# Kernel optimization log

Measured on AMD Instinct MI355X. Metric: run time of the kernel, lower is better.

Reference implementation:

```python
import jax, jax.numpy as jnp
import numpy as np

ALPHA = 1.0  # DPMConfig.alpha
N, D, K = 4096, 256, 64


def setup_inputs() -> dict:
    key = jax.random.key(0)
    k1, k2, k3, k4 = jax.random.split(key, 4)
    x = jax.random.normal(k1, (N, D), dtype=jnp.float32)
    means = jax.random.normal(k2, (K, D), dtype=jnp.float32)
    # SPD covariances: A A^T / D + 0.5 I
    A = jax.random.normal(k3, (K, D, D), dtype=jnp.float32)
    covs = jnp.einsum('kde,kfe->kdf', A, A) / D + 0.5 * jnp.eye(D, dtype=jnp.float32)
    counts = jax.random.uniform(k4, (K,), dtype=jnp.float32, minval=1.0, maxval=200.0)
    n_points = 100000
    return {"x": x, "means": means, "covs": covs, "counts": counts, "n_points": n_points}


def reference(x, means, covs, counts, n_points):
    n, d = x.shape
    k = means.shape[0]
    # deviations from every cluster mean: [N, K, D]
    dev = x[:, None, :] - means[None, :, :]
    # batched Mahalanobis solve: covs broadcast over points
    solved = jnp.linalg.solve(covs[None], dev[..., None])[..., 0]  # [N, K, D]
    quad = jnp.sum(dev * solved, axis=-1)  # [N, K]
    # logdet with the same jitter as the original
    _, log_dets = jnp.linalg.slogdet(covs + 1e-10 * jnp.eye(d, dtype=covs.dtype))  # [K]
    log_lik = -0.5 * (d * jnp.log(2.0 * jnp.pi) + log_dets[None, :] + quad)  # [N, K]
    denom = jnp.asarray(n_points, jnp.float32) + ALPHA
    log_prior = jnp.log(counts / denom)  # [K]
    log_new = jnp.log(ALPHA / denom)
    log_probs = jnp.concatenate(
        [log_lik + log_prior[None, :], jnp.full((n, 1), log_new, dtype=x.dtype)], axis=1
    )  # [N, K+1]
    # stable normalize (max-subtract + exp + sum == softmax)
    probs = jax.nn.softmax(log_probs, axis=1)
    return probs
```

## Files before the change

### kernel.cpp

```cpp
#include <hip/hip_runtime.h>
#include <math.h>


#define DD 256
#define KC 64
#define NPTS 4096
#define NT 64
#define BB 64
#define KG 4

__global__ __launch_bounds__(512) void pivot_kernel(
    const float* __restrict__ covs, float* __restrict__ S,
    float* __restrict__ Plbuf, float* __restrict__ ldp, int bs)
{
  const int k = blockIdx.x;
  const int by = blockIdx.y;
  const int tid = threadIdx.x;
  float* Pb = Plbuf + (size_t)k * BB * BB;

  __shared__ __align__(16) float Tl[BB][BB + 4];
  __shared__ __align__(16) float pivc[2][BB];
  __shared__ __align__(16) float pivr[2][BB];

  if (by < 4) {
    if (bs == 0) return;
    const int j0p = (bs - 1) * BB;
    const int r0 = by * BB;
    const float* src = ((bs == 1) ? covs : (const float*)S) + (size_t)k * DD * DD;
    float* dst = S + (size_t)k * DD * DD;

    const int rr = tid >> 3;
    const int cc = (tid & 7) * 8;
    *reinterpret_cast<float4*>(&Tl[rr][cc]) =
        *reinterpret_cast<const float4*>(&Pb[rr * BB + cc]);
    *reinterpret_cast<float4*>(&Tl[rr][cc + 4]) =
        *reinterpret_cast<const float4*>(&Pb[rr * BB + cc + 4]);
    __syncthreads();

    const int r = r0 + rr;
    if (r0 == j0p) {
      *reinterpret_cast<float4*>(&dst[(size_t)r * DD + j0p + cc]) =
          *reinterpret_cast<const float4*>(&Tl[rr][cc]);
      *reinterpret_cast<float4*>(&dst[(size_t)r * DD + j0p + cc + 4]) =
          *reinterpret_cast<const float4*>(&Tl[rr][cc + 4]);
    } else {
      float Crow[BB];
      #pragma unroll
      for (int p = 0; p < BB; p += 4) {
        float4 cv = *reinterpret_cast<const float4*>(&src[(size_t)r * DD + j0p + p]);
        Crow[p] = cv.x; Crow[p + 1] = cv.y; Crow[p + 2] = cv.z; Crow[p + 3] = cv.w;
      }
      float acc[8] = {0.f, 0.f, 0.f, 0.f, 0.f, 0.f, 0.f, 0.f};
      #pragma unroll
      for (int p = 0; p < BB; ++p) {
        float4 t0 = *reinterpret_cast<const float4*>(&Tl[p][cc]);
        float4 t1 = *reinterpret_cast<const float4*>(&Tl[p][cc + 4]);
        acc[0] = fmaf(Crow[p], t0.x, acc[0]);
        acc[1] = fmaf(Crow[p], t0.y, acc[1]);
        acc[2] = fmaf(Crow[p], t0.z, acc[2]);
        acc[3] = fmaf(Crow[p], t0.w, acc[3]);
        acc[4] = fmaf(Crow[p], t1.x, acc[4]);
        acc[5] = fmaf(Crow[p], t1.y, acc[5]);
        acc[6] = fmaf(Crow[p], t1.z, acc[6]);
        acc[7] = fmaf(Crow[p], t1.w, acc[7]);
      }
      float4 o0 = {-acc[0], -acc[1], -acc[2], -acc[3]};
      float4 o1 = {-acc[4], -acc[5], -acc[6], -acc[7]};
      *reinterpret_cast<float4*>(&dst[(size_t)r * DD + j0p + cc]) = o0;
      *reinterpret_cast<float4*>(&dst[(size_t)r * DD + j0p + cc + 4]) = o1;
    }
    return;
  }

  if (bs == 4) return;

  const int j0 = bs * BB;
  const float* psrc = ((bs == 0) ? covs : (const float*)S) + (size_t)k * DD * DD;
  const int pr = tid >> 3;
  const int pc = (tid & 7) * 8;

  float v[8];
  {
    float4 a4 = *reinterpret_cast<const float4*>(&psrc[(size_t)(j0 + pr) * DD + j0 + pc]);
    float4 b4 = *reinterpret_cast<const float4*>(&psrc[(size_t)(j0 + pr) * DD + j0 + pc + 4]);
    v[0] = a4.x; v[1] = a4.y; v[2] = a4.z; v[3] = a4.w;
    v[4] = b4.x; v[5] = b4.y; v[6] = b4.z; v[7] = b4.w;
  }
  if (pc == 0) pivc[0][pr] = v[0];
  if (pr == 0) {
    #pragma unroll
    for (int e = 0; e < 8; ++e) pivr[0][pc + e] = v[e];
  }
  __syncthreads();

  float ld = 0.0f;
  #pragma unroll 1
  for (int p = 0; p < BB; ++p) {
    const int cur = p & 1, nxt = cur ^ 1;
    const float d = pivc[cur][p];
    const float inv_d = 1.0f / d;
    if (tid == 0) ld += logf(d);
    const float cr = pivc[cur][pr];
    float rw[8];
    *reinterpret_cast<float4*>(&rw[0]) = *reinterpret_cast<const float4*>(&pivr[cur][pc]);
    *reinterpret_cast<float4*>(&rw[4]) = *reinterpret_cast<const float4*>(&pivr[cur][pc + 4]);
    #pragma unroll
    for (int e = 0; e < 8; ++e) {
      float ge = fmaf(-inv_d * cr, rw[e], v[e]);
      if (pr == p)     ge = rw[e] * inv_d;
      if (pc + e == p) ge = (pr == p) ? -inv_d : cr * inv_d;
      v[e] = ge;
    }
    if (p < BB - 1) {
      if (pr == p + 1) {
        #pragma unroll
        for (int e = 0; e < 8; ++e) pivr[nxt][pc + e] = v[e];
      }
      if (pc <= p + 1 && p + 1 < pc + 8) pivc[nxt][pr] = v[p + 1 - pc];
    }
    __syncthreads();
  }

  float4 s0 = {v[0], v[1], v[2], v[3]};
  float4 s1 = {v[4], v[5], v[6], v[7]};
  *reinterpret_cast<float4*>(&Pb[pr * BB + pc]) = s0;
  *reinterpret_cast<float4*>(&Pb[pr * BB + pc + 4]) = s1;
  if (tid == 0) ldp[bs * KC + k] = ld;
}

__global__ __launch_bounds__(512) void update_kernel(
    const float* __restrict__ covs, float* __restrict__ S,
    const float* __restrict__ Plbuf, int bs)
{
  const int k = blockIdx.x;
  const int si = blockIdx.y;
  const int t = si + (si >= bs ? 1 : 0);
  const int c0 = t * BB;
  const int j0 = bs * BB;
  const int tid = threadIdx.x;
  const float* src = ((bs == 0) ? covs : (const float*)S) + (size_t)k * DD * DD;
  float* dst = S + (size_t)k * DD * DD;

  __shared__ __align__(16) float Pl[BB][BB + 4];
  __shared__ __align__(16) float SJ[BB][BB + 4];
  __shared__ __align__(16) float Tl[BB][BB + 4];

  const float* Pb = Plbuf + (size_t)k * BB * BB;
  #pragma unroll
  for (int q = 0; q < 8; ++q) {
    int e = q * 512 + tid;
    int r = e >> 6, c = e & 63;
    Pl[r][c] = Pb[e];
    SJ[r][c] = src[(size_t)(j0 + r) * DD + c0 + c];
  }
  __syncthreads();

  {
    const int c = tid & 63;
    const int rg = (tid >> 6) * 8;
    float tv[8];
    #pragma unroll
    for (int r = 0; r < 8; ++r) tv[r] = 0.0f;
    for (int p = 0; p < BB; p += 4) {
      float s0 = SJ[p][c], s1 = SJ[p + 1][c], s2 = SJ[p + 2][c], s3 = SJ[p + 3][c];
      #pragma unroll
      for (int r = 0; r < 8; ++r) {
        float4 pv = *reinterpret_cast<const float4*>(&Pl[rg + r][p]);
        tv[r] = fmaf(pv.x, s0, fmaf(pv.y, s1, fmaf(pv.z, s2, fmaf(pv.w, s3, tv[r]))));
      }
    }
    #pragma unroll
    for (int r = 0; r < 8; ++r) Tl[rg + r][c] = tv[r];
  }
  __syncthreads();

  const int r = tid & 255;
  const int h = (tid >> 8) * 32;
  const bool inJ = (r >= j0) && (r < j0 + BB);
  if (inJ) {
    #pragma unroll
    for (int c = 0; c < 32; c += 4) {
      float4 tv4 = *reinterpret_cast<const float4*>(&Tl[r - j0][h + c]);
      float4 o = {-tv4.x, -tv4.y, -tv4.z, -tv4.w};
      *reinterpret_cast<float4*>(&dst[(size_t)r * DD + c0 + h + c]) = o;
    }
  } else {
    float Crow[BB];
    #pragma unroll
    for (int p = 0; p < BB; p += 4) {
      float4 cv = *reinterpret_cast<const float4*>(&src[(size_t)r * DD + j0 + p]);
      Crow[p] = cv.x; Crow[p + 1] = cv.y; Crow[p + 2] = cv.z; Crow[p + 3] = cv.w;
    }
    #pragma unroll
    for (int c = 0; c < 32; c += 4) {
      float4 acc = *reinterpret_cast<const float4*>(&src[(size_t)r * DD + c0 + h + c]);
      #pragma unroll
      for (int p = 0; p < BB; ++p) {
        float4 tv4 = *reinterpret_cast<const float4*>(&Tl[p][h + c]);
        acc.x = fmaf(Crow[p], tv4.x, acc.x);
        acc.y = fmaf(Crow[p], tv4.y, acc.y);
        acc.z = fmaf(Crow[p], tv4.z, acc.z);
        acc.w = fmaf(Crow[p], tv4.w, acc.w);
      }
      *reinterpret_cast<float4*>(&dst[(size_t)r * DD + c0 + h + c]) = acc;
    }
  }
}

__global__ __launch_bounds__(256) void w_kernel(
    const float* __restrict__ S, const float* __restrict__ means,
    const float* __restrict__ counts, const int* __restrict__ n_points_p,
    const float* __restrict__ ldp, float* __restrict__ cA,
    float* __restrict__ wv)
{
  const int k = blockIdx.x;
  const int tid = threadIdx.x;
  if (tid == 0) {
    float denom = (float)(*n_points_p) + 1.0f;
    float ld = ldp[k] + ldp[KC + k] + ldp[2 * KC + k] + ldp[3 * KC + k];
    cA[k] = logf(counts[k] / denom) - 0.5f * (470.49652900079047f + ld);
  }
  const float* Sk = S + (size_t)k * DD * DD;
  __shared__ float mus[DD];
  mus[tid] = means[(size_t)k * DD + tid];
  __syncthreads();
  float a0 = 0.f, a1 = 0.f, a2 = 0.f, a3 = 0.f;
  for (int j = 0; j < DD; j += 4) {
    a0 = fmaf(Sk[(size_t)(j + 0) * DD + tid], mus[j + 0], a0);
    a1 = fmaf(Sk[(size_t)(j + 1) * DD + tid], mus[j + 1], a1);
    a2 = fmaf(Sk[(size_t)(j + 2) * DD + tid], mus[j + 2], a2);
    a3 = fmaf(Sk[(size_t)(j + 3) * DD + tid], mus[j + 3], a3);
  }
  wv[(size_t)k * DD + tid] = (a0 + a1) + (a2 + a3);
}

__global__ __launch_bounds__(256) void quad_kernel(
    const float* __restrict__ X, const float* __restrict__ means,
    const float* __restrict__ S, const float* __restrict__ cA,
    const float* __restrict__ wv, float* __restrict__ lp)
{
  __shared__ __align__(16) float XT[DD][NT];
  __shared__ __align__(16) float qred[32 * NT];
  __shared__ __align__(16) float muw[2][DD];
  __shared__ __align__(16) float lpb[KG][NT];

  const int tid = threadIdx.x;
  const int n0 = blockIdx.x * NT;
  const int k0 = blockIdx.y * KG;

  #pragma unroll
  for (int q = 0; q < 16; ++q) {
    int f = q * 1024 + tid * 4;
    int r = f >> 8;
    int c = f & 255;
    float4 xv = *reinterpret_cast<const float4*>(X + (size_t)(n0 + r) * DD + c);
    int rs = r ^ (((c >> 2) & 15) << 2);
    XT[c + 0][rs] = xv.x;
    XT[c + 1][rs] = xv.y;
    XT[c + 2][rs] = xv.z;
    XT[c + 3][rs] = xv.w;
  }

  const int tn = tid & 7;
  const int tj = tid >> 3;

  #pragma unroll 1
  for (int kk = 0; kk < KG; ++kk) {
    const int k = k0 + kk;
    const float* Skc = S + (size_t)k * DD * DD + tj * 8;

    __syncthreads();
    muw[0][tid] = means[(size_t)k * DD + tid];
    muw[1][tid] = wv[(size_t)k * DD + tid];

    float y[8][8];
    #pragma unroll
    for (int a = 0; a < 8; ++a)
      #pragma unroll
      for (int b = 0; b < 8; ++b) y[a][b] = 0.0f;

    float pA[8], pB[8];
    *reinterpret_cast<float4*>(&pA[0]) = *reinterpret_cast<const float4*>(Skc + 0);
    *reinterpret_cast<float4*>(&pA[4]) = *reinterpret_cast<const float4*>(Skc + 4);
    #pragma unroll 1
    for (int i = 0; i < DD; i += 2) {
      const float* nb = Skc + (size_t)(i + 1) * DD;
      *reinterpret_cast<float4*>(&pB[0]) = *reinterpret_cast<const float4*>(nb + 0);
      *reinterpret_cast<float4*>(&pB[4]) = *reinterpret_cast<const float4*>(nb + 4);
      {
        const int sw = ((i >> 2) & 15) << 2;
        float xv[8];
        *reinterpret_cast<float4*>(&xv[0]) =
            *reinterpret_cast<const float4*>(&XT[i][(tn * 8) ^ sw]);
        *reinterpret_cast<float4*>(&xv[4]) =
            *reinterpret_cast<const float4*>(&XT[i][(tn * 8 + 4) ^ sw]);
        #pragma unroll
        for (int a = 0; a < 8; ++a)
          #pragma unroll
          for (int b = 0; b < 8; ++b)
            y[a][b] = fmaf(xv[a], pA[b], y[a][b]);
      }
      const float* na = Skc + (size_t)((i + 2 < DD) ? (i + 2) : i) * DD;
      *reinterpret_cast<float4*>(&pA[0]) = *reinterpret_cast<const float4*>(na + 0);
      *reinterpret_cast<float4*>(&pA[4]) = *reinterpret_cast<const float4*>(na + 4);
      {
        const int i1 = i + 1;
        const int sw = ((i1 >> 2) & 15) << 2;
        float xv[8];
        *reinterpret_cast<float4*>(&xv[0]) =
            *reinterpret_cast<const float4*>(&XT[i1][(tn * 8) ^ sw]);
        *reinterpret_cast<float4*>(&xv[4]) =
            *reinterpret_cast<const float4*>(&XT[i1][(tn * 8 + 4) ^ sw]);
        #pragma unroll
        for (int a = 0; a < 8; ++a)
          #pragma unroll
          for (int b = 0; b < 8; ++b)
            y[a][b] = fmaf(xv[a], pB[b], y[a][b]);
      }
    }
    __syncthreads();

    float s[8];
    #pragma unroll
    for (int a = 0; a < 8; ++a) s[a] = 0.0f;
    #pragma unroll
    for (int b = 0; b < 8; ++b) {
      const int j = tj * 8 + b;
      const int swj = ((j >> 2) & 15) << 2;
      float dv[8];
      *reinterpret_cast<float4*>(&dv[0]) =
          *reinterpret_cast<const float4*>(&XT[j][(tn * 8) ^ swj]);
      *reinterpret_cast<float4*>(&dv[4]) =
          *reinterpret_cast<const float4*>(&XT[j][(tn * 8 + 4) ^ swj]);
      const float mj = muw[0][j];
      const float wj = muw[1][j];
      #pragma unroll
      for (int a = 0; a < 8; ++a)
        s[a] = fmaf(dv[a] - mj, y[a][b] - wj, s[a]);
    }

    *reinterpret_cast<float4*>(&qred[tj * 64 + tn * 8]) =
        *reinterpret_cast<const float4*>(&s[0]);
    *reinterpret_cast<float4*>(&qred[tj * 64 + tn * 8 + 4]) =
        *reinterpret_cast<const float4*>(&s[4]);
    __syncthreads();
    if (tid < 64) {
      float qa = 0.f, qb = 0.f, qc = 0.f, qd = 0.f;
      #pragma unroll
      for (int t = 0; t < 32; t += 4) {
        qa += qred[(t + 0) * 64 + tid];
        qb += qred[(t + 1) * 64 + tid];
        qc += qred[(t + 2) * 64 + tid];
        qd += qred[(t + 3) * 64 + tid];
      }
      lpb[kk][tid] = fmaf(0.5f, (qa + qb) + (qc + qd), cA[k]);
    }
  }

  __syncthreads();
  if (tid < 64) {
    float4 o = {lpb[0][tid], lpb[1][tid], lpb[2][tid], lpb[3][tid]};
    *reinterpret_cast<float4*>(&lp[(size_t)(n0 + tid) * KC + k0]) = o;
  }
}

__global__ __launch_bounds__(64) void softmax_kernel(
    const float* __restrict__ lp, const int* __restrict__ n_points_p,
    float* __restrict__ out)
{
  const int n = blockIdx.x;
  const int l = threadIdx.x;
  const float denom = (float)(*n_points_p) + 1.0f;
  const float log_new = -logf(denom);

  float v = lp[(size_t)n * KC + l];
  float m = v;
  #pragma unroll
  for (int off = 32; off > 0; off >>= 1) m = fmaxf(m, __shfl_xor(m, off, 64));
  m = fmaxf(m, log_new);

  float e = expf(v - m);
  float s = e;
  #pragma unroll
  for (int off = 32; off > 0; off >>= 1) s += __shfl_xor(s, off, 64);
  float enew = expf(log_new - m);
  s += enew;

  out[(size_t)n * (KC + 1) + l] = e / s;
  if (l == 0) out[(size_t)n * (KC + 1) + KC] = enew / s;
}

extern "C" void kernel_launch(void* const* d_in, const int* in_sizes, int n_in,
                              void* d_out, int out_size, void* d_ws, size_t ws_size,
                              hipStream_t stream)
{
  const float* x       = (const float*)d_in[0];
  const float* means   = (const float*)d_in[1];
  const float* covs    = (const float*)d_in[2];
  const float* counts  = (const float*)d_in[3];
  const int*   n_points = (const int*)d_in[4];

  float* S   = (float*)d_ws;
  float* cA  = S + (size_t)KC * DD * DD;
  float* ldp = cA + KC;
  float* lp  = ldp + 4 * KC;
  float* Plbuf = lp;
  float* out = (float*)d_out;
  float* wv = out;

  for (int bs = 0; bs < 4; ++bs) {
    pivot_kernel<<<dim3(KC, 5), 512, 0, stream>>>(covs, S, Plbuf, ldp, bs);
    update_kernel<<<dim3(KC, 3), 512, 0, stream>>>(covs, S, Plbuf, bs);
  }
  pivot_kernel<<<dim3(KC, 5), 512, 0, stream>>>(covs, S, Plbuf, ldp, 4);
  w_kernel<<<KC, 256, 0, stream>>>(S, means, counts, n_points, ldp, cA, wv);
  quad_kernel<<<dim3(NPTS / NT, KC / KG), 256, 0, stream>>>(x, means, S, cA, wv, lp);
  softmax_kernel<<<NPTS, 64, 0, stream>>>(lp, n_points, out);
}
```

Measured before the change: 694.4 us.

## Stage even rows of S through shared memory in quad kernel

The quad kernel's inner product loop now splits the rows of the S matrix by parity. Even rows are loaded cooperatively into a small shared-memory tile with a one-step register prefetch. Odd rows are still streamed directly from global memory into double-buffered registers. The aim is to halve the per-thread global load traffic and latency on the critical FMA loop, at the cost of two block barriers per 8-row chunk and extra shared-memory reads.

```diff
diff --git a/kernel.cpp b/kernel.cpp
--- a/kernel.cpp
+++ b/kernel.cpp
@@ -240,9 +240,10 @@
     const float* __restrict__ wv, float* __restrict__ lp)
 {
   __shared__ __align__(16) float XT[DD][NT];
-  __shared__ __align__(16) float qred[32 * NT];
+  __shared__ __align__(16) float Pl[4 * DD];
   __shared__ __align__(16) float muw[2][DD];
   __shared__ __align__(16) float lpb[KG][NT];
+  __shared__ __align__(16) float qred[32 * NT];
 
   const int tid = threadIdx.x;
   const int n0 = blockIdx.x * NT;
@@ -263,62 +264,93 @@
 
   const int tn = tid & 7;
   const int tj = tid >> 3;
+  const int sq = tid >> 6;
+  const int sc = (tid * 4) & 255;
 
   #pragma unroll 1
   for (int kk = 0; kk < KG; ++kk) {
     const int k = k0 + kk;
-    const float* Skc = S + (size_t)k * DD * DD + tj * 8;
+    const float* Sk = S + (size_t)k * DD * DD;
+    const float* Skj = Sk + tj * 8;
 
     __syncthreads();
     muw[0][tid] = means[(size_t)k * DD + tid];
     muw[1][tid] = wv[(size_t)k * DD + tid];
 
+    float4 pre = *reinterpret_cast<const float4*>(Sk + (size_t)(2 * sq) * DD + sc);
+    float ov0[8], ov1[8];
+    *reinterpret_cast<float4*>(&ov0[0]) = *reinterpret_cast<const float4*>(Skj + 1 * DD);
+    *reinterpret_cast<float4*>(&ov0[4]) = *reinterpret_cast<const float4*>(Skj + 1 * DD + 4);
+    *reinterpret_cast<float4*>(&ov1[0]) = *reinterpret_cast<const float4*>(Skj + 3 * DD);
+    *reinterpret_cast<float4*>(&ov1[4]) = *reinterpret_cast<const float4*>(Skj + 3 * DD + 4);
+
     float y[8][8];
     #pragma unroll
     for (int a = 0; a < 8; ++a)
       #pragma unroll
       for (int b = 0; b < 8; ++b) y[a][b] = 0.0f;
 
-    float pA[8], pB[8];
-    *reinterpret_cast<float4*>(&pA[0]) = *reinterpret_cast<const float4*>(Skc + 0);
-    *reinterpret_cast<float4*>(&pA[4]) = *reinterpret_cast<const float4*>(Skc + 4);
     #pragma unroll 1
-    for (int i = 0; i < DD; i += 2) {
-      const float* nb = Skc + (size_t)(i + 1) * DD;
-      *reinterpret_cast<float4*>(&pB[0]) = *reinterpret_cast<const float4*>(nb + 0);
-      *reinterpret_cast<float4*>(&pB[4]) = *reinterpret_cast<const float4*>(nb + 4);
-      {
-        const int sw = ((i >> 2) & 15) << 2;
-        float xv[8];
-        *reinterpret_cast<float4*>(&xv[0]) =
-            *reinterpret_cast<const float4*>(&XT[i][(tn * 8) ^ sw]);
-        *reinterpret_cast<float4*>(&xv[4]) =
-            *reinterpret_cast<const float4*>(&XT[i][(tn * 8 + 4) ^ sw]);
-        #pragma unroll
-        for (int a = 0; a < 8; ++a)
+    for (int ct = 0; ct < 32; ++ct) {
+      __syncthreads();
+      *reinterpret_cast<float4*>(&Pl[tid * 4]) = pre;
+      if (ct < 31) {
+        pre = *reinterpret_cast<const float4*>(
+            Sk + (size_t)((ct + 1) * 8 + 2 * sq) * DD + sc);
+      }
+      __syncthreads();
+
+      #pragma unroll
+      for (int q = 0; q < 4; ++q) {
+        const int ie = ct * 8 + 2 * q;
+        {
+          const int sw = ((ie >> 2) & 15) << 2;
+          float xv[8], pv[8];
+          *reinterpret_cast<float4*>(&xv[0]) =
+              *reinterpret_cast<const float4*>(&XT[ie][(tn * 8) ^ sw]);
+          *reinterpret_cast<float4*>(&xv[4]) =
+              *reinterpret_cast<const float4*>(&XT[ie][(tn * 8 + 4) ^ sw]);
+          *reinterpret_cast<float4*>(&pv[0]) =
+              *reinterpret_cast<const float4*>(&Pl[q * DD + tj * 8]);
+          *reinterpret_cast<float4*>(&pv[4]) =
+              *reinterpret_cast<const float4*>(&Pl[q * DD + tj * 8 + 4]);
           #pragma unroll
-          for (int b = 0; b < 8; ++b)
-            y[a][b] = fmaf(xv[a], pA[b], y[a][b]);
-      }
-      const float* na = Skc + (size_t)((i + 2 < DD) ? (i + 2) : i) * DD;
-      *reinterpret_cast<float4*>(&pA[0]) = *reinterpret_cast<const float4*>(na + 0);
-      *reinterpret_cast<float4*>(&pA[4]) = *reinterpret_cast<const float4*>(na + 4);
-      {
-        const int i1 = i + 1;
-        const int sw = ((i1 >> 2) & 15) << 2;
-        float xv[8];
-        *reinterpret_cast<float4*>(&xv[0]) =
-            *reinterpret_cast<const float4*>(&XT[i1][(tn * 8) ^ sw]);
-        *reinterpret_cast<float4*>(&xv[4]) =
-            *reinterpret_cast<const float4*>(&XT[i1][(tn * 8 + 4) ^ sw]);
-        #pragma unroll
-        for (int a = 0; a < 8; ++a)
-          #pragma unroll
-          for (int b = 0; b < 8; ++b)
-            y[a][b] = fmaf(xv[a], pB[b], y[a][b]);
-      }
-    }
-    __syncthreads();
+          for (int a = 0; a < 8; ++a)
+            #pragma unroll
+            for (int b = 0; b < 8; ++b)
+              y[a][b] = fmaf(xv[a], pv[b], y[a][b]);
+        }
+        {
+          const int io = ie + 1;
+          const int sw = ((io >> 2) & 15) << 2;
+          float xv[8];
+          *reinterpret_cast<float4*>(&xv[0]) =
+              *reinterpret_cast<const float4*>(&XT[io][(tn * 8) ^ sw]);
+          *reinterpret_cast<float4*>(&xv[4]) =
+              *reinterpret_cast<const float4*>(&XT[io][(tn * 8 + 4) ^ sw]);
+          int inx = io + 4;
+          if (inx > 255) inx = 255;
+          const float* np = Skj + (size_t)inx * DD;
+          if ((q & 1) == 0) {
+            #pragma unroll
+            for (int a = 0; a < 8; ++a)
+              #pragma unroll
+              for (int b = 0; b < 8; ++b)
+                y[a][b] = fmaf(xv[a], ov0[b], y[a][b]);
+            *reinterpret_cast<float4*>(&ov0[0]) = *reinterpret_cast<const float4*>(np);
+            *reinterpret_cast<float4*>(&ov0[4]) = *reinterpret_cast<const float4*>(np + 4);
+          } else {
+            #pragma unroll
+            for (int a = 0; a < 8; ++a)
+              #pragma unroll
+              for (int b = 0; b < 8; ++b)
+                y[a][b] = fmaf(xv[a], ov1[b], y[a][b]);
+            *reinterpret_cast<float4*>(&ov1[0]) = *reinterpret_cast<const float4*>(np);
+            *reinterpret_cast<float4*>(&ov1[4]) = *reinterpret_cast<const float4*>(np + 4);
+          }
+        }
+      }
+    }
 
     float s[8];
     #pragma unroll
```

Measured after the change: 670.6 us. 1.04x faster.
